# Kernel tuning notes

Measured on AMD Instinct MI355X. Metric: run time of the kernel, lower is better.

## Reference

```python
import jax, jax.numpy as jnp
import numpy as np
from jax import lax

K = 4
H = 1024
IN = 512
OUT = 8192
T = 128
B = 32


def setup_inputs() -> dict:
    key = jax.random.key(0)
    ks = jax.random.split(key, 5)
    return {
        "X": jax.random.normal(ks[0], (T, B, IN), dtype=jnp.float32),
        "Wxh_w": jax.random.normal(ks[1], (H, IN), dtype=jnp.float32) * 0.02,
        "Wxh_b": jax.random.normal(ks[2], (H,), dtype=jnp.float32) * 0.02,
        "Whh_w": jax.random.normal(ks[3], (H, (K - 1) * H), dtype=jnp.float32) * 0.02,
        "Wmo_w": jax.random.normal(ks[4], (OUT, K * H), dtype=jnp.float32) * 0.02,
    }


def reference(X, Wxh_w, Wxh_b, Whh_w, Wmo_w):
    batch = X.shape[1]
    # history stack hs: [K-1, B, H], hs[0] = oldest, hs[-1] = newest
    hs0 = jnp.zeros((K - 1, batch, H), dtype=X.dtype)

    def step(hs, x_t):
        # concat reversed(h_prevs): newest block first -> [B, (K-1)*H]
        h_cat = hs[::-1].transpose(1, 0, 2).reshape(batch, (K - 1) * H)
        h_t = jax.nn.selu(x_t @ Wxh_w.T + Wxh_b + h_cat @ Whh_w.T)  # [B, H]
        h_out = jnp.concatenate([h_t, h_cat], axis=1)  # [B, K*H]
        out_t = h_out @ Wmo_w.T  # [B, OUT]
        new_hs = jnp.concatenate([hs[1:], h_t[None]], axis=0)
        # truncated BPTT: detach the (new) oldest hidden
        new_hs = new_hs.at[0].set(lax.stop_gradient(new_hs[0]))
        return new_hs, out_t

    _, outs = lax.scan(step, hs0, X)
    return outs  # [T, B, OUT]
```

## Files before the change

### kernel.cpp

```cpp
#include <hip/hip_runtime.h>
#include <hip/hip_bf16.h>

#define T_STEPS 128
#define BATCH   32
#define IN_DIM  512
#define H_DIM   1024
#define OUT_DIM 8192
#define KH      3072
#define NWG     128
#define SLOT_E  32768
#define NSLOT   131

typedef __attribute__((ext_vector_type(8))) short short8;
typedef __attribute__((ext_vector_type(4))) float f32x4;

__device__ __forceinline__ unsigned short bf16_rne(float f) {
  unsigned u = __float_as_uint(f);
  unsigned r = (u + 0x7FFFu + ((u >> 16) & 1u)) >> 16;
  return (unsigned short)r;
}

__device__ __forceinline__ void gload_lds16(const void* g, void* l) {
  __builtin_amdgcn_global_load_lds(
      (const __attribute__((address_space(1))) void*)g,
      (__attribute__((address_space(3))) void*)l, 16, 0, 0);
}

__global__ __launch_bounds__(256) void convert_kernel(
    const float* __restrict__ src, unsigned short* __restrict__ dst, int n4) {
  int i = blockIdx.x * blockDim.x + threadIdx.x;
  const int stride = gridDim.x * blockDim.x;
  for (; i < n4; i += stride) {
    float4 v = ((const float4*)src)[i];
    ushort4 o;
    o.x = bf16_rne(v.x); o.y = bf16_rne(v.y);
    o.z = bf16_rne(v.z); o.w = bf16_rne(v.w);
    ((ushort4*)dst)[i] = o;
  }
}

__global__ __launch_bounds__(256) void pre_kernel(
    const float* __restrict__ X, const float* __restrict__ Wxh,
    const float* __restrict__ bias, float* __restrict__ preT) {
  __shared__ float xs[32][260];
  const int tid = threadIdx.x;
  const int t  = blockIdx.x >> 4;
  const int jb = blockIdx.x & 15;
  const int b  = tid & 31;
  const int jg = tid >> 5;
  float acc[8];
  #pragma unroll
  for (int i = 0; i < 8; ++i) acc[i] = 0.f;

  for (int kc = 0; kc < 2; ++kc) {
    __syncthreads();
    #pragma unroll
    for (int v = tid; v < 2048; v += 256) {
      int br = v >> 6, i4 = v & 63;
      float4 x4 = *(const float4*)(X + (size_t)t*(BATCH*IN_DIM) + (size_t)br*IN_DIM + kc*256 + i4*4);
      *(float4*)&xs[br][i4*4] = x4;
    }
    __syncthreads();
    for (int i = 0; i < 256; i += 4) {
      const int k = kc*256 + i;
      float4 xv = *(const float4*)&xs[b][i];
      #pragma unroll
      for (int jj = 0; jj < 8; ++jj) {
        const int j = jb*64 + jg + jj*8;
        float4 w4 = *(const float4*)(Wxh + (size_t)j*IN_DIM + k);
        acc[jj] += xv.x*w4.x + xv.y*w4.y + xv.z*w4.z + xv.w*w4.w;
      }
    }
  }
  #pragma unroll
  for (int jj = 0; jj < 8; ++jj) {
    const int j = jb*64 + jg + jj*8;
    preT[(size_t)t*(H_DIM*BATCH) + (size_t)j*BATCH + b] = acc[jj] + bias[j];
  }
}

template<int RN, int RD1, int RD2>
__device__ __forceinline__ void do_step(
    const int t, const int tid, const int wg, const int j0,
    const int lane, const int wv,
    const short8* __restrict__ wf, const short8* __restrict__ hi8,
    const short8* __restrict__ lo8, const float* __restrict__ preT,
    unsigned short* __restrict__ hHi, unsigned short* __restrict__ hLo,
    int* __restrict__ grp, int* __restrict__ rootcnt, int* __restrict__ rootrep,
    short8 (&Rh0)[3][4], short8 (&Rh1)[3][4],
    short8 (&Rl0)[3][4], short8 (&Rl1)[3][4],
    float (&red)[8][16][33],
    unsigned short (&hpk_hi)[32][8], unsigned short (&hpk_lo)[32][8]) {
  f32x4 a0h = {}, a0l = {}, a1h = {}, a1l = {};

  #pragma unroll
  for (int i = 0; i < 4; ++i) {
    const int ks = 32 + wv*4 + i;
    const short8 af = wf[ks*64 + lane];
    a0h = __builtin_amdgcn_mfma_f32_16x16x32_bf16(af, Rh0[RD1][i], a0h, 0, 0, 0);
    a1h = __builtin_amdgcn_mfma_f32_16x16x32_bf16(af, Rh1[RD1][i], a1h, 0, 0, 0);
    a0l = __builtin_amdgcn_mfma_f32_16x16x32_bf16(af, Rl0[RD1][i], a0l, 0, 0, 0);
    a1l = __builtin_amdgcn_mfma_f32_16x16x32_bf16(af, Rl1[RD1][i], a1l, 0, 0, 0);
  }
  #pragma unroll
  for (int i = 0; i < 4; ++i) {
    const int ks = 64 + wv*4 + i;
    const short8 af = wf[ks*64 + lane];
    a0h = __builtin_amdgcn_mfma_f32_16x16x32_bf16(af, Rh0[RD2][i], a0h, 0, 0, 0);
    a1h = __builtin_amdgcn_mfma_f32_16x16x32_bf16(af, Rh1[RD2][i], a1h, 0, 0, 0);
    a0l = __builtin_amdgcn_mfma_f32_16x16x32_bf16(af, Rl0[RD2][i], a0l, 0, 0, 0);
    a1l = __builtin_amdgcn_mfma_f32_16x16x32_bf16(af, Rl1[RD2][i], a1l, 0, 0, 0);
  }

  float upre = 0.f;
  if (tid < 256)
    upre = preT[(size_t)t*(H_DIM*BATCH) + (size_t)(j0 + (tid >> 5))*BATCH + (tid & 31)];

  if (t > 0) {
    if (tid == 0) {
      while (!__hip_atomic_load(&rootrep[(((t-1) << 3) + (wg & 7)) << 4],
                                __ATOMIC_RELAXED, __HIP_MEMORY_SCOPE_AGENT))
        __builtin_amdgcn_s_sleep(2);
    }
    __syncthreads();
    asm volatile("" ::: "memory");
  }

  {
    const size_t sb = (size_t)(128 - t) * 4096;
    #pragma unroll
    for (int i = 0; i < 4; ++i) {
      const int ks = wv*4 + i;
      const size_t bidx = sb + (size_t)ks*128 + (size_t)(lane >> 4)*32 + (lane & 15);
      Rh0[RN][i] = hi8[bidx];
      Rh1[RN][i] = hi8[bidx + 16];
      Rl0[RN][i] = lo8[bidx];
      Rl1[RN][i] = lo8[bidx + 16];
    }
  }
  #pragma unroll
  for (int i = 0; i < 4; ++i) {
    const int ks = wv*4 + i;
    const short8 af = wf[ks*64 + lane];
    a0h = __builtin_amdgcn_mfma_f32_16x16x32_bf16(af, Rh0[RN][i], a0h, 0, 0, 0);
    a1h = __builtin_amdgcn_mfma_f32_16x16x32_bf16(af, Rh1[RN][i], a1h, 0, 0, 0);
    a0l = __builtin_amdgcn_mfma_f32_16x16x32_bf16(af, Rl0[RN][i], a0l, 0, 0, 0);
    a1l = __builtin_amdgcn_mfma_f32_16x16x32_bf16(af, Rl1[RN][i], a1l, 0, 0, 0);
  }

  const f32x4 s0 = a0h + a0l;
  const f32x4 s1 = a1h + a1l;
  const int rr = (lane >> 4) * 4, cc = lane & 15;
  #pragma unroll
  for (int q = 0; q < 4; ++q) {
    red[wv][rr + q][cc]      = s0[q];
    red[wv][rr + q][16 + cc] = s1[q];
  }
  __syncthreads();

  if (tid < 256) {
    const int jj = tid >> 5, b = tid & 31;
    float u = upre;
    #pragma unroll
    for (int w = 0; w < 8; ++w)
      u += red[w][jj][b] + red[w][jj + 8][b];
    const float h = u > 0.f ? 1.0507009873554805f*u
                            : (1.0507009873554805f*1.6732632423543772f)*expm1f(u);
    const unsigned short hh = bf16_rne(h);
    hpk_hi[b][jj] = hh;
    hpk_lo[b][jj] = bf16_rne(h - __uint_as_float((unsigned)hh << 16));
  }
  __syncthreads();

  if (tid < 32) {
    const int b = tid;
    const size_t base = (size_t)(127 - t)*SLOT_E + (size_t)(j0 >> 3)*256 + (size_t)b*8;
    const unsigned long long h0 = *(const unsigned long long*)&hpk_hi[b][0];
    const unsigned long long h1 = *(const unsigned long long*)&hpk_hi[b][4];
    const unsigned long long l0 = *(const unsigned long long*)&hpk_lo[b][0];
    const unsigned long long l1 = *(const unsigned long long*)&hpk_lo[b][4];
    __hip_atomic_store((unsigned long long*)(hHi + base),     h0, __ATOMIC_RELAXED, __HIP_MEMORY_SCOPE_AGENT);
    __hip_atomic_store((unsigned long long*)(hHi + base) + 1, h1, __ATOMIC_RELAXED, __HIP_MEMORY_SCOPE_AGENT);
    __hip_atomic_store((unsigned long long*)(hLo + base),     l0, __ATOMIC_RELAXED, __HIP_MEMORY_SCOPE_AGENT);
    __hip_atomic_store((unsigned long long*)(hLo + base) + 1, l1, __ATOMIC_RELAXED, __HIP_MEMORY_SCOPE_AGENT);
    if (t < T_STEPS - 1) {
      asm volatile("s_waitcnt vmcnt(0)" ::: "memory");
      if (tid == 0) {
        const int g = wg >> 3;
        if (__hip_atomic_fetch_add(&grp[((t << 4) + g) << 4], 1, __ATOMIC_RELAXED, __HIP_MEMORY_SCOPE_AGENT) == 7) {
          if (__hip_atomic_fetch_add(&rootcnt[t << 4], 1, __ATOMIC_RELAXED, __HIP_MEMORY_SCOPE_AGENT) == 15) {
            #pragma unroll
            for (int r = 0; r < 8; ++r)
              __hip_atomic_store(&rootrep[((t << 3) + r) << 4], 1,
                                 __ATOMIC_RELAXED, __HIP_MEMORY_SCOPE_AGENT);
          }
        }
      }
    }
  }
}

__global__ __launch_bounds__(512, 2) void recur_kernel(
    const float* __restrict__ Whh, const float* __restrict__ preT,
    unsigned short* __restrict__ hHi, unsigned short* __restrict__ hLo,
    int* __restrict__ grp, int* __restrict__ rootcnt, int* __restrict__ rootrep) {
  __shared__ __align__(16) unsigned short w_lds[96*64*8];
  __shared__ float red[8][16][33];
  __shared__ __align__(16) unsigned short hpk_hi[32][8];
  __shared__ __align__(16) unsigned short hpk_lo[32][8];
  const int tid  = threadIdx.x;
  const int wg   = blockIdx.x;
  const int j0   = wg * 8;
  const int lane = tid & 63;
  const int wv   = tid >> 6;

  for (int s = tid; s < 6144; s += 512) {
    const int ks = s >> 6, l = s & 63;
    const int r = l & 15;
    const int j = j0 + (r & 7);
    const int part = r >> 3;
    const int kb = ks*32 + (l >> 4)*8;
    const float* wp = Whh + (size_t)j*KH + kb;
    unsigned short tmp[8];
    #pragma unroll
    for (int i = 0; i < 8; ++i) {
      const float f = wp[i];
      unsigned short v = bf16_rne(f);
      if (part) v = bf16_rne(f - __uint_as_float((unsigned)v << 16));
      tmp[i] = v;
    }
    *(short8*)&w_lds[s*8] = *(short8*)tmp;
  }
  __syncthreads();

  const short8* wf  = (const short8*)w_lds;
  const short8* hi8 = (const short8*)hHi;
  const short8* lo8 = (const short8*)hLo;

  short8 Rh0[3][4], Rh1[3][4], Rl0[3][4], Rl1[3][4];
  const short8 z8 = {};
  #pragma unroll
  for (int r = 1; r < 3; ++r)
    #pragma unroll
    for (int i = 0; i < 4; ++i) {
      Rh0[r][i] = z8; Rh1[r][i] = z8; Rl0[r][i] = z8; Rl1[r][i] = z8;
    }

  for (int t3 = 0; t3 < 126; t3 += 3) {
    do_step<0,2,1>(t3,   tid, wg, j0, lane, wv, wf, hi8, lo8, preT, hHi, hLo,
                   grp, rootcnt, rootrep, Rh0, Rh1, Rl0, Rl1, red, hpk_hi, hpk_lo);
    do_step<1,0,2>(t3+1, tid, wg, j0, lane, wv, wf, hi8, lo8, preT, hHi, hLo,
                   grp, rootcnt, rootrep, Rh0, Rh1, Rl0, Rl1, red, hpk_hi, hpk_lo);
    do_step<2,1,0>(t3+2, tid, wg, j0, lane, wv, wf, hi8, lo8, preT, hHi, hLo,
                   grp, rootcnt, rootrep, Rh0, Rh1, Rl0, Rl1, red, hpk_hi, hpk_lo);
  }
  do_step<0,2,1>(126, tid, wg, j0, lane, wv, wf, hi8, lo8, preT, hHi, hLo,
                 grp, rootcnt, rootrep, Rh0, Rh1, Rl0, Rl1, red, hpk_hi, hpk_lo);
  do_step<1,0,2>(127, tid, wg, j0, lane, wv, wf, hi8, lo8, preT, hHi, hLo,
                 grp, rootcnt, rootrep, Rh0, Rh1, Rl0, Rl1, red, hpk_hi, hpk_lo);
}

__global__ __launch_bounds__(256) void gemm_kernel(
    const unsigned short* __restrict__ Ah, const unsigned short* __restrict__ Bm,
    float* __restrict__ C) {
  __shared__ __align__(16) unsigned short lA[2][4096];
  __shared__ __align__(16) unsigned short lB[2][4096];
  const int tid = threadIdx.x;
  const int wg = blockIdx.x;
  const int x = wg & 7;
  const int c = wg >> 3;
  const int mb = (x >> 2)*16 + (c & 15);
  const int nb = (x & 3)*16 + (c >> 4);
  const int lane = tid & 63;
  const int wv = tid >> 6;
  const int wm = wv >> 1, wn = wv & 1;
  const int lrow = lane & 15, lhalf = lane >> 4;
  const int rowB0 = tid >> 2, qB = tid & 3;
  f32x4 acc[4][4] = {};

#define STAGE(buf, kt) do {                                                    \
    _Pragma("unroll")                                                          \
    for (int it = 0; it < 2; ++it) {                                           \
      const int idxA = it*4 + wv;                                              \
      const int tA = mb*4 + (idxA >> 1);                                       \
      gload_lds16(Ah + (size_t)(127 - tA)*SLOT_E + (size_t)(kt)*1024           \
                     + (idxA & 1)*512 + (size_t)lane*8,                        \
                  &lA[buf][idxA*512]);                                         \
      const int rB = it*64 + rowB0;                                            \
      const int qs = qB ^ ((rB ^ (rB >> 2)) & 3);                              \
      gload_lds16(Bm + (size_t)(nb*128 + rB)*4096 + (size_t)(kt)*32 + qs*8,    \
                  &lB[buf][(tid & 192)*8 + it*2048]);                          \
    } } while (0)

  STAGE(0, 0);
  for (int kt = 0; kt < 128; ++kt) {
    const int cur = kt & 1;
    if (kt < 127) {
      STAGE(cur ^ 1, kt + 1);
      asm volatile("s_waitcnt vmcnt(4)" ::: "memory");
    } else {
      asm volatile("s_waitcnt vmcnt(0)" ::: "memory");
    }
    __syncthreads();
    short8 af[4], bf[4];
    #pragma unroll
    for (int mi = 0; mi < 4; ++mi) {
      const int tg = wm*2 + (mi >> 1);
      af[mi] = *(const short8*)&lA[cur][tg*1024 + lhalf*256 + (lrow + (mi & 1)*16)*8];
    }
    #pragma unroll
    for (int ni = 0; ni < 4; ++ni) {
      const int r = wn*64 + ni*16 + lrow;
      const int qs = lhalf ^ ((r ^ (r >> 2)) & 3);
      bf[ni] = *(const short8*)&lB[cur][r*32 + qs*8];
    }
    #pragma unroll
    for (int mi = 0; mi < 4; ++mi)
      #pragma unroll
      for (int ni = 0; ni < 4; ++ni)
        acc[mi][ni] = __builtin_amdgcn_mfma_f32_16x16x32_bf16(af[mi], bf[ni], acc[mi][ni], 0, 0, 0);
    __syncthreads();
  }
#undef STAGE

  const int orow0 = mb*128 + wm*64 + lhalf*4;
  const int ocol0 = nb*128 + wn*64 + lrow;
  #pragma unroll
  for (int mi = 0; mi < 4; ++mi)
    #pragma unroll
    for (int ni = 0; ni < 4; ++ni)
      #pragma unroll
      for (int q = 0; q < 4; ++q)
        __builtin_nontemporal_store(acc[mi][ni][q],
            &C[(size_t)(orow0 + mi*16 + q)*OUT_DIM + ocol0 + ni*16]);
}

extern "C" void kernel_launch(void* const* d_in, const int* in_sizes, int n_in,
                              void* d_out, int out_size, void* d_ws, size_t ws_size,
                              hipStream_t stream) {
  (void)in_sizes; (void)n_in; (void)out_size; (void)ws_size;
  const float* X   = (const float*)d_in[0];
  const float* Wxh = (const float*)d_in[1];
  const float* Wxb = (const float*)d_in[2];
  const float* Whh = (const float*)d_in[3];
  const float* Wmo = (const float*)d_in[4];
  float* out = (float*)d_out;
  char* ws = (char*)d_ws;

  const size_t OFF_PRET = 0;
  const size_t OFF_HHI  = OFF_PRET + (size_t)T_STEPS*H_DIM*BATCH*4;
  const size_t OFF_HLO  = OFF_HHI + (size_t)NSLOT*SLOT_E*2;
  const size_t OFF_GRP  = OFF_HLO + (size_t)NSLOT*SLOT_E*2;
  const size_t OFF_RCNT = OFF_GRP + (size_t)T_STEPS*16*64;
  const size_t OFF_RREP = OFF_RCNT + (size_t)T_STEPS*64;
  const size_t OFF_W16  = OFF_RREP + (size_t)T_STEPS*8*64;

  float* preT = (float*)(ws + OFF_PRET);
  unsigned short* hHi = (unsigned short*)(ws + OFF_HHI);
  unsigned short* hLo = (unsigned short*)(ws + OFF_HLO);
  int* grp     = (int*)(ws + OFF_GRP);
  int* rootcnt = (int*)(ws + OFF_RCNT);
  int* rootrep = (int*)(ws + OFF_RREP);
  unsigned short* Wmo16 = (unsigned short*)(ws + OFF_W16);

  hipMemsetAsync(hHi + (size_t)128*SLOT_E, 0, (size_t)3*SLOT_E*2, stream);
  hipMemsetAsync(hLo + (size_t)128*SLOT_E, 0, (size_t)3*SLOT_E*2, stream);
  hipMemsetAsync(grp, 0, (size_t)T_STEPS*16*64 + (size_t)T_STEPS*64 + (size_t)T_STEPS*8*64, stream);

  convert_kernel<<<2048, 256, 0, stream>>>(Wmo, Wmo16, (int)((size_t)OUT_DIM*4096/4));
  pre_kernel<<<2048, 256, 0, stream>>>(X, Wxh, Wxb, preT);
  recur_kernel<<<NWG, 512, 0, stream>>>(Whh, preT, hHi, hLo, grp, rootcnt, rootrep);
  gemm_kernel<<<2048, 256, 0, stream>>>(hHi, Wmo16, out);
}
```

Before: 1.133 ms.

## Fuse recurrence and output GEMM into persistent kernel with ticketed tile consumption

Merges the recurrent kernel and the output projection GEMM into one persistent kernel of 256 workgroups. Idle workgroups, and recurrent workgroups once they finish, pull GEMM tiles from an atomic ticket counter and spin on the per-timestep rootrep flags, so output tiles for early timesteps are computed while the recurrence is still running. The change also removes the last-step exemption from signalling, moves the GEMM to 512 threads per tile, and shares LDS between the two phases. Risks include contention between GEMM loads and the latency-critical recurrence, lower occupancy with one block per CU, and the cost of spin-waiting.

```diff
diff --git a/kernel.cpp b/kernel.cpp
--- a/kernel.cpp
+++ b/kernel.cpp
@@ -10,6 +10,7 @@
 #define NWG     128
 #define SLOT_E  32768
 #define NSLOT   131
+#define NTILE   2048
 
 typedef __attribute__((ext_vector_type(8))) short short8;
 typedef __attribute__((ext_vector_type(4))) float f32x4;
@@ -89,8 +90,8 @@
     int* __restrict__ grp, int* __restrict__ rootcnt, int* __restrict__ rootrep,
     short8 (&Rh0)[3][4], short8 (&Rh1)[3][4],
     short8 (&Rl0)[3][4], short8 (&Rl1)[3][4],
-    float (&red)[8][16][33],
-    unsigned short (&hpk_hi)[32][8], unsigned short (&hpk_lo)[32][8]) {
+    float (*red)[16][33],
+    unsigned short (*hpk_hi)[8], unsigned short (*hpk_lo)[8]) {
   f32x4 a0h = {}, a0l = {}, a1h = {}, a1l = {};
 
   #pragma unroll
@@ -183,156 +184,167 @@
     __hip_atomic_store((unsigned long long*)(hHi + base) + 1, h1, __ATOMIC_RELAXED, __HIP_MEMORY_SCOPE_AGENT);
     __hip_atomic_store((unsigned long long*)(hLo + base),     l0, __ATOMIC_RELAXED, __HIP_MEMORY_SCOPE_AGENT);
     __hip_atomic_store((unsigned long long*)(hLo + base) + 1, l1, __ATOMIC_RELAXED, __HIP_MEMORY_SCOPE_AGENT);
-    if (t < T_STEPS - 1) {
-      asm volatile("s_waitcnt vmcnt(0)" ::: "memory");
-      if (tid == 0) {
-        const int g = wg >> 3;
-        if (__hip_atomic_fetch_add(&grp[((t << 4) + g) << 4], 1, __ATOMIC_RELAXED, __HIP_MEMORY_SCOPE_AGENT) == 7) {
-          if (__hip_atomic_fetch_add(&rootcnt[t << 4], 1, __ATOMIC_RELAXED, __HIP_MEMORY_SCOPE_AGENT) == 15) {
-            #pragma unroll
-            for (int r = 0; r < 8; ++r)
-              __hip_atomic_store(&rootrep[((t << 3) + r) << 4], 1,
-                                 __ATOMIC_RELAXED, __HIP_MEMORY_SCOPE_AGENT);
-          }
+    asm volatile("s_waitcnt vmcnt(0)" ::: "memory");
+    if (tid == 0) {
+      const int g = wg >> 3;
+      if (__hip_atomic_fetch_add(&grp[((t << 4) + g) << 4], 1, __ATOMIC_RELAXED, __HIP_MEMORY_SCOPE_AGENT) == 7) {
+        if (__hip_atomic_fetch_add(&rootcnt[t << 4], 1, __ATOMIC_RELAXED, __HIP_MEMORY_SCOPE_AGENT) == 15) {
+          #pragma unroll
+          for (int r = 0; r < 8; ++r)
+            __hip_atomic_store(&rootrep[((t << 3) + r) << 4], 1,
+                               __ATOMIC_RELAXED, __HIP_MEMORY_SCOPE_AGENT);
         }
       }
     }
   }
 }
 
-__global__ __launch_bounds__(512, 2) void recur_kernel(
+__device__ __forceinline__ void gemm_consume(
+    const unsigned short* __restrict__ Ah, const unsigned short* __restrict__ Bm,
+    float* __restrict__ C, int* __restrict__ ticket, int* __restrict__ rootrep,
+    const int wg, const int tid,
+    unsigned short (*lA)[4096], unsigned short (*lB)[4096], int* tk_ls) {
+  const int lane = tid & 63;
+  const int wv = tid >> 6;
+  const int wm = wv >> 2, wn = wv & 3;
+  const int lrow = lane & 15, lhalf = lane >> 4;
+  const int rB = tid >> 2, qB = tid & 3;
+  const int qsB = qB ^ ((rB ^ (rB >> 2)) & 3);
+
+  for (;;) {
+    if (tid == 0)
+      *tk_ls = __hip_atomic_fetch_add(ticket, 1, __ATOMIC_RELAXED, __HIP_MEMORY_SCOPE_AGENT);
+    __syncthreads();
+    const int tk = *tk_ls;
+    if (tk >= NTILE) return;
+    const int mb = tk >> 6, nb = tk & 63;
+
+    if (tid == 0) {
+      while (!__hip_atomic_load(&rootrep[(((4*mb + 3) << 3) + (wg & 7)) << 4],
+                                __ATOMIC_RELAXED, __HIP_MEMORY_SCOPE_AGENT))
+        __builtin_amdgcn_s_sleep(2);
+    }
+    __syncthreads();
+    asm volatile("" ::: "memory");
+
+    f32x4 acc[4][2] = {};
+    const int tA = mb*4 + (wv >> 1);
+    const unsigned short* aSrc = Ah + (size_t)(127 - tA)*SLOT_E + (wv & 1)*512 + (size_t)lane*8;
+    const unsigned short* bSrc = Bm + (size_t)(nb*128 + rB)*4096 + (size_t)qsB*8;
+
+    gload_lds16(aSrc, &lA[0][wv*512]);
+    gload_lds16(bSrc, &lB[0][wv*512]);
+    for (int kt = 0; kt < 128; ++kt) {
+      const int cur = kt & 1;
+      if (kt < 127) {
+        gload_lds16(aSrc + (size_t)(kt+1)*1024, &lA[cur ^ 1][wv*512]);
+        gload_lds16(bSrc + (size_t)(kt+1)*32,   &lB[cur ^ 1][wv*512]);
+        asm volatile("s_waitcnt vmcnt(2)" ::: "memory");
+      } else {
+        asm volatile("s_waitcnt vmcnt(0)" ::: "memory");
+      }
+      __syncthreads();
+      short8 afr[4], bfr[2];
+      #pragma unroll
+      for (int mi = 0; mi < 4; ++mi) {
+        const int tg = wm*2 + (mi >> 1);
+        afr[mi] = *(const short8*)&lA[cur][tg*1024 + lhalf*256 + ((mi & 1)*16 + lrow)*8];
+      }
+      #pragma unroll
+      for (int ni = 0; ni < 2; ++ni) {
+        const int r = wn*32 + ni*16 + lrow;
+        const int qs = lhalf ^ ((r ^ (r >> 2)) & 3);
+        bfr[ni] = *(const short8*)&lB[cur][r*32 + qs*8];
+      }
+      #pragma unroll
+      for (int mi = 0; mi < 4; ++mi)
+        #pragma unroll
+        for (int ni = 0; ni < 2; ++ni)
+          acc[mi][ni] = __builtin_amdgcn_mfma_f32_16x16x32_bf16(afr[mi], bfr[ni], acc[mi][ni], 0, 0, 0);
+      __syncthreads();
+    }
+    const int orow0 = mb*128 + wm*64 + lhalf*4;
+    const int ocol0 = nb*128 + wn*32 + lrow;
+    #pragma unroll
+    for (int mi = 0; mi < 4; ++mi)
+      #pragma unroll
+      for (int ni = 0; ni < 2; ++ni)
+        #pragma unroll
+        for (int q = 0; q < 4; ++q)
+          __builtin_nontemporal_store(acc[mi][ni][q],
+              &C[(size_t)(orow0 + mi*16 + q)*OUT_DIM + ocol0 + ni*16]);
+  }
+}
+
+__global__ __launch_bounds__(512, 1) void fused_kernel(
     const float* __restrict__ Whh, const float* __restrict__ preT,
     unsigned short* __restrict__ hHi, unsigned short* __restrict__ hLo,
-    int* __restrict__ grp, int* __restrict__ rootcnt, int* __restrict__ rootrep) {
-  __shared__ __align__(16) unsigned short w_lds[96*64*8];
-  __shared__ float red[8][16][33];
-  __shared__ __align__(16) unsigned short hpk_hi[32][8];
-  __shared__ __align__(16) unsigned short hpk_lo[32][8];
-  const int tid  = threadIdx.x;
-  const int wg   = blockIdx.x;
-  const int j0   = wg * 8;
-  const int lane = tid & 63;
-  const int wv   = tid >> 6;
-
-  for (int s = tid; s < 6144; s += 512) {
-    const int ks = s >> 6, l = s & 63;
-    const int r = l & 15;
-    const int j = j0 + (r & 7);
-    const int part = r >> 3;
-    const int kb = ks*32 + (l >> 4)*8;
-    const float* wp = Whh + (size_t)j*KH + kb;
-    unsigned short tmp[8];
-    #pragma unroll
-    for (int i = 0; i < 8; ++i) {
-      const float f = wp[i];
-      unsigned short v = bf16_rne(f);
-      if (part) v = bf16_rne(f - __uint_as_float((unsigned)v << 16));
-      tmp[i] = v;
-    }
-    *(short8*)&w_lds[s*8] = *(short8*)tmp;
-  }
-  __syncthreads();
-
-  const short8* wf  = (const short8*)w_lds;
-  const short8* hi8 = (const short8*)hHi;
-  const short8* lo8 = (const short8*)hLo;
-
-  short8 Rh0[3][4], Rh1[3][4], Rl0[3][4], Rl1[3][4];
-  const short8 z8 = {};
-  #pragma unroll
-  for (int r = 1; r < 3; ++r)
-    #pragma unroll
-    for (int i = 0; i < 4; ++i) {
-      Rh0[r][i] = z8; Rh1[r][i] = z8; Rl0[r][i] = z8; Rl1[r][i] = z8;
-    }
-
-  for (int t3 = 0; t3 < 126; t3 += 3) {
-    do_step<0,2,1>(t3,   tid, wg, j0, lane, wv, wf, hi8, lo8, preT, hHi, hLo,
+    int* __restrict__ grp, int* __restrict__ rootcnt, int* __restrict__ rootrep,
+    int* __restrict__ ticket, const unsigned short* __restrict__ Wmo16,
+    float* __restrict__ C) {
+  __shared__ __align__(16) char smem[116224];
+  __shared__ int tk_ls;
+  const int tid = threadIdx.x;
+  const int wg  = blockIdx.x;
+  unsigned short* w_lds = (unsigned short*)smem;
+  float (*red)[16][33] = (float (*)[16][33])(smem + 98304);
+  unsigned short (*hpk_hi)[8] = (unsigned short (*)[8])(smem + 115200);
+  unsigned short (*hpk_lo)[8] = (unsigned short (*)[8])(smem + 115712);
+  unsigned short (*lA)[4096] = (unsigned short (*)[4096])(smem);
+  unsigned short (*lB)[4096] = (unsigned short (*)[4096])(smem + 16384);
+
+  if (wg < NWG) {
+    const int j0   = wg * 8;
+    const int lane = tid & 63;
+    const int wv   = tid >> 6;
+
+    for (int s = tid; s < 6144; s += 512) {
+      const int ks = s >> 6, l = s & 63;
+      const int r = l & 15;
+      const int j = j0 + (r & 7);
+      const int part = r >> 3;
+      const int kb = ks*32 + (l >> 4)*8;
+      const float* wp = Whh + (size_t)j*KH + kb;
+      unsigned short tmp[8];
+      #pragma unroll
+      for (int i = 0; i < 8; ++i) {
+        const float f = wp[i];
+        unsigned short v = bf16_rne(f);
+        if (part) v = bf16_rne(f - __uint_as_float((unsigned)v << 16));
+        tmp[i] = v;
+      }
+      *(short8*)&w_lds[s*8] = *(short8*)tmp;
+    }
+    __syncthreads();
+
+    const short8* wf  = (const short8*)w_lds;
+    const short8* hi8 = (const short8*)hHi;
+    const short8* lo8 = (const short8*)hLo;
+
+    short8 Rh0[3][4], Rh1[3][4], Rl0[3][4], Rl1[3][4];
+    const short8 z8 = {};
+    #pragma unroll
+    for (int r = 1; r < 3; ++r)
+      #pragma unroll
+      for (int i = 0; i < 4; ++i) {
+        Rh0[r][i] = z8; Rh1[r][i] = z8; Rl0[r][i] = z8; Rl1[r][i] = z8;
+      }
+
+    for (int t3 = 0; t3 < 126; t3 += 3) {
+      do_step<0,2,1>(t3,   tid, wg, j0, lane, wv, wf, hi8, lo8, preT, hHi, hLo,
+                     grp, rootcnt, rootrep, Rh0, Rh1, Rl0, Rl1, red, hpk_hi, hpk_lo);
+      do_step<1,0,2>(t3+1, tid, wg, j0, lane, wv, wf, hi8, lo8, preT, hHi, hLo,
+                     grp, rootcnt, rootrep, Rh0, Rh1, Rl0, Rl1, red, hpk_hi, hpk_lo);
+      do_step<2,1,0>(t3+2, tid, wg, j0, lane, wv, wf, hi8, lo8, preT, hHi, hLo,
+                     grp, rootcnt, rootrep, Rh0, Rh1, Rl0, Rl1, red, hpk_hi, hpk_lo);
+    }
+    do_step<0,2,1>(126, tid, wg, j0, lane, wv, wf, hi8, lo8, preT, hHi, hLo,
                    grp, rootcnt, rootrep, Rh0, Rh1, Rl0, Rl1, red, hpk_hi, hpk_lo);
-    do_step<1,0,2>(t3+1, tid, wg, j0, lane, wv, wf, hi8, lo8, preT, hHi, hLo,
+    do_step<1,0,2>(127, tid, wg, j0, lane, wv, wf, hi8, lo8, preT, hHi, hLo,
                    grp, rootcnt, rootrep, Rh0, Rh1, Rl0, Rl1, red, hpk_hi, hpk_lo);
-    do_step<2,1,0>(t3+2, tid, wg, j0, lane, wv, wf, hi8, lo8, preT, hHi, hLo,
-                   grp, rootcnt, rootrep, Rh0, Rh1, Rl0, Rl1, red, hpk_hi, hpk_lo);
-  }
-  do_step<0,2,1>(126, tid, wg, j0, lane, wv, wf, hi8, lo8, preT, hHi, hLo,
-                 grp, rootcnt, rootrep, Rh0, Rh1, Rl0, Rl1, red, hpk_hi, hpk_lo);
-  do_step<1,0,2>(127, tid, wg, j0, lane, wv, wf, hi8, lo8, preT, hHi, hLo,
-                 grp, rootcnt, rootrep, Rh0, Rh1, Rl0, Rl1, red, hpk_hi, hpk_lo);
-}
-
-__global__ __launch_bounds__(256) void gemm_kernel(
-    const unsigned short* __restrict__ Ah, const unsigned short* __restrict__ Bm,
-    float* __restrict__ C) {
-  __shared__ __align__(16) unsigned short lA[2][4096];
-  __shared__ __align__(16) unsigned short lB[2][4096];
-  const int tid = threadIdx.x;
-  const int wg = blockIdx.x;
-  const int x = wg & 7;
-  const int c = wg >> 3;
-  const int mb = (x >> 2)*16 + (c & 15);
-  const int nb = (x & 3)*16 + (c >> 4);
-  const int lane = tid & 63;
-  const int wv = tid >> 6;
-  const int wm = wv >> 1, wn = wv & 1;
-  const int lrow = lane & 15, lhalf = lane >> 4;
-  const int rowB0 = tid >> 2, qB = tid & 3;
-  f32x4 acc[4][4] = {};
-
-#define STAGE(buf, kt) do {                                                    \
-    _Pragma("unroll")                                                          \
-    for (int it = 0; it < 2; ++it) {                                           \
-      const int idxA = it*4 + wv;                                              \
-      const int tA = mb*4 + (idxA >> 1);                                       \
-      gload_lds16(Ah + (size_t)(127 - tA)*SLOT_E + (size_t)(kt)*1024           \
-                     + (idxA & 1)*512 + (size_t)lane*8,                        \
-                  &lA[buf][idxA*512]);                                         \
-      const int rB = it*64 + rowB0;                                            \
-      const int qs = qB ^ ((rB ^ (rB >> 2)) & 3);                              \
-      gload_lds16(Bm + (size_t)(nb*128 + rB)*4096 + (size_t)(kt)*32 + qs*8,    \
-                  &lB[buf][(tid & 192)*8 + it*2048]);                          \
-    } } while (0)
-
-  STAGE(0, 0);
-  for (int kt = 0; kt < 128; ++kt) {
-    const int cur = kt & 1;
-    if (kt < 127) {
-      STAGE(cur ^ 1, kt + 1);
-      asm volatile("s_waitcnt vmcnt(4)" ::: "memory");
-    } else {
-      asm volatile("s_waitcnt vmcnt(0)" ::: "memory");
-    }
-    __syncthreads();
-    short8 af[4], bf[4];
-    #pragma unroll
-    for (int mi = 0; mi < 4; ++mi) {
-      const int tg = wm*2 + (mi >> 1);
-      af[mi] = *(const short8*)&lA[cur][tg*1024 + lhalf*256 + (lrow + (mi & 1)*16)*8];
-    }
-    #pragma unroll
-    for (int ni = 0; ni < 4; ++ni) {
-      const int r = wn*64 + ni*16 + lrow;
-      const int qs = lhalf ^ ((r ^ (r >> 2)) & 3);
-      bf[ni] = *(const short8*)&lB[cur][r*32 + qs*8];
-    }
-    #pragma unroll
-    for (int mi = 0; mi < 4; ++mi)
-      #pragma unroll
-      for (int ni = 0; ni < 4; ++ni)
-        acc[mi][ni] = __builtin_amdgcn_mfma_f32_16x16x32_bf16(af[mi], bf[ni], acc[mi][ni], 0, 0, 0);
-    __syncthreads();
-  }
-#undef STAGE
-
-  const int orow0 = mb*128 + wm*64 + lhalf*4;
-  const int ocol0 = nb*128 + wn*64 + lrow;
-  #pragma unroll
-  for (int mi = 0; mi < 4; ++mi)
-    #pragma unroll
-    for (int ni = 0; ni < 4; ++ni)
-      #pragma unroll
-      for (int q = 0; q < 4; ++q)
-        __builtin_nontemporal_store(acc[mi][ni][q],
-            &C[(size_t)(orow0 + mi*16 + q)*OUT_DIM + ocol0 + ni*16]);
+    __syncthreads();
+  }
+  gemm_consume(hHi, Wmo16, C, ticket, rootrep, wg, tid, lA, lB, &tk_ls);
 }
 
 extern "C" void kernel_launch(void* const* d_in, const int* in_sizes, int n_in,
@@ -353,7 +365,8 @@
   const size_t OFF_GRP  = OFF_HLO + (size_t)NSLOT*SLOT_E*2;
   const size_t OFF_RCNT = OFF_GRP + (size_t)T_STEPS*16*64;
   const size_t OFF_RREP = OFF_RCNT + (size_t)T_STEPS*64;
-  const size_t OFF_W16  = OFF_RREP + (size_t)T_STEPS*8*64;
+  const size_t OFF_TKT  = OFF_RREP + (size_t)T_STEPS*8*64;
+  const size_t OFF_W16  = OFF_TKT + 64;
 
   float* preT = (float*)(ws + OFF_PRET);
   unsigned short* hHi = (unsigned short*)(ws + OFF_HHI);
@@ -361,14 +374,16 @@
   int* grp     = (int*)(ws + OFF_GRP);
   int* rootcnt = (int*)(ws + OFF_RCNT);
   int* rootrep = (int*)(ws + OFF_RREP);
+  int* ticket  = (int*)(ws + OFF_TKT);
   unsigned short* Wmo16 = (unsigned short*)(ws + OFF_W16);
 
   hipMemsetAsync(hHi + (size_t)128*SLOT_E, 0, (size_t)3*SLOT_E*2, stream);
   hipMemsetAsync(hLo + (size_t)128*SLOT_E, 0, (size_t)3*SLOT_E*2, stream);
-  hipMemsetAsync(grp, 0, (size_t)T_STEPS*16*64 + (size_t)T_STEPS*64 + (size_t)T_STEPS*8*64, stream);
+  hipMemsetAsync(grp, 0, (size_t)T_STEPS*16*64 + (size_t)T_STEPS*64
+                        + (size_t)T_STEPS*8*64 + 64, stream);
 
   convert_kernel<<<2048, 256, 0, stream>>>(Wmo, Wmo16, (int)((size_t)OUT_DIM*4096/4));
   pre_kernel<<<2048, 256, 0, stream>>>(X, Wxh, Wxb, preT);
-  recur_kernel<<<NWG, 512, 0, stream>>>(Whh, preT, hHi, hLo, grp, rootcnt, rootrep);
-  gemm_kernel<<<2048, 256, 0, stream>>>(hHi, Wmo16, out);
-}
+  fused_kernel<<<256, 512, 0, stream>>>(Whh, preT, hHi, hLo, grp, rootcnt,
+                                        rootrep, ticket, Wmo16, out);
+}
```

After: 1.282 ms. 13.1% more time.
